# Performance work log

Measured on AMD Instinct MI355X. Metric: run time of the kernel, lower is better.

Reference implementation:

```python
import jax, jax.numpy as jnp
import numpy as np


def setup_inputs() -> dict:
    key = jax.random.key(0)
    ks = jax.random.split(key, 8)
    h = 256
    b, o, T = 64, 64, 50
    s = 1.0 / np.sqrt(h)  # torch LSTM/Linear default init scale
    return {
        "x": jax.random.normal(ks[0], (b, o, h), dtype=jnp.float32),
        "W_ih": jax.random.uniform(ks[1], (4 * h, h), jnp.float32, -s, s),
        "W_hh": jax.random.uniform(ks[2], (4 * h, h), jnp.float32, -s, s),
        "b_ih": jax.random.uniform(ks[3], (4 * h,), jnp.float32, -s, s),
        "b_hh": jax.random.uniform(ks[4], (4 * h,), jnp.float32, -s, s),
        "c0": jnp.zeros((1, h), dtype=jnp.float32),
        "W_out": jax.random.uniform(ks[5], (h, h), jnp.float32, -s, s),
        "b_out": jax.random.uniform(ks[6], (h,), jnp.float32, -s, s),
        "sequence_length": T,
    }


def reference(x, W_ih, W_hh, b_ih, b_hh, c0, W_out, b_out, sequence_length):
    b, o, f = x.shape
    B = b * o
    h0 = x.reshape(B, f)                       # initial hidden state = input
    c_init = jnp.broadcast_to(c0, (B, f))      # learned initial cell state
    # Input token is constant across time: precompute input projection once.
    x_proj = h0 @ W_ih.T + b_ih + b_hh         # (B, 4f)

    def step(carry, _):
        hp, cp = carry
        gates = x_proj + hp @ W_hh.T           # (B, 4f), torch gate order i,f,g,o
        i_g, f_g, g_g, o_g = jnp.split(gates, 4, axis=-1)
        i_g = jax.nn.sigmoid(i_g)
        f_g = jax.nn.sigmoid(f_g)
        g_g = jnp.tanh(g_g)
        o_g = jax.nn.sigmoid(o_g)
        c = f_g * cp + i_g * g_g
        hn = o_g * jnp.tanh(c)
        return (hn, c), hn

    (_, _), hs = jax.lax.scan(step, (h0, c_init), None, length=sequence_length)
    # hs: (T, B, f) -> (b, o, T, f)
    hs = hs.transpose(1, 0, 2).reshape(b, o, sequence_length, f)
    return hs @ W_out.T + b_out
```

## Files before the change

### kernel.cpp

```cpp
#include <hip/hip_runtime.h>

typedef __attribute__((ext_vector_type(8))) short short8;
typedef __attribute__((ext_vector_type(4))) float f32x4;

#define F   256
#define SH  264

__device__ __forceinline__ short f2bf(float f) {
    union { float f; unsigned u; } v; v.f = f;
    unsigned r = (v.u + 0x7fffu + ((v.u >> 16) & 1u)) >> 16;
    return (short)r;
}
__device__ __forceinline__ float bf2f(short s) {
    union { float f; unsigned u; } v; v.u = ((unsigned)(unsigned short)s) << 16;
    return v.f;
}
__device__ __forceinline__ float sigm(float x) {
    return __builtin_amdgcn_rcpf(1.f + __builtin_amdgcn_exp2f(-1.442695041f * x));
}
__device__ __forceinline__ float tanhx(float x) {
    return 1.f - 2.f * __builtin_amdgcn_rcpf(1.f + __builtin_amdgcn_exp2f(2.885390082f * x));
}
__device__ __forceinline__ f32x4 splat4(float v) {
    f32x4 r; r[0] = v; r[1] = v; r[2] = v; r[3] = v; return r;
}

__global__ void pack_kernel(const float* __restrict__ Whh, const float* __restrict__ Wih,
                            const float* __restrict__ Wout,
                            short* __restrict__ whh_p, short* __restrict__ wih_hi,
                            short* __restrict__ wih_lo, short* __restrict__ wout_p)
{
    int idx = blockIdx.x * blockDim.x + threadIdx.x;
    if (idx < 64 * 8 * 64) {
        int lane = idx & 63, kt = (idx >> 6) & 7, nt = idx >> 9;
        int n = nt * 16 + (lane & 15);
        int k = kt * 32 + (lane >> 4) * 8;
        const float* s1 = Whh + n * F + k;
        const float* s2 = Wih + n * F + k;
        #pragma unroll
        for (int j = 0; j < 8; j++) {
            whh_p[idx * 8 + j] = f2bf(s1[j]);
            float v = s2[j];
            short hi = f2bf(v);
            wih_hi[idx * 8 + j] = hi;
            wih_lo[idx * 8 + j] = f2bf(v - bf2f(hi));
        }
    } else {
        int i2 = idx - 64 * 8 * 64;
        if (i2 < 16 * 8 * 64) {
            int lane = i2 & 63, kt = (i2 >> 6) & 7, nt = i2 >> 9;
            int n = nt * 16 + (lane & 15);
            int k = kt * 32 + (lane >> 4) * 8;
            const float* s = Wout + n * F + k;
            #pragma unroll
            for (int j = 0; j < 8; j++) wout_p[i2 * 8 + j] = f2bf(s[j]);
        }
    }
}

__device__ __forceinline__ void gate_mm(f32x4 (&acc)[8][2], const short* __restrict__ Wp,
                                        const short* hb, int w, int lane)
{
    const int l15 = lane & 15, quad = lane >> 4;
    #pragma unroll
    for (int kt = 0; kt < 8; kt++) {
        short8 a0 = *(const short8*)(hb + l15 * SH + kt * 32 + quad * 8);
        short8 a1 = *(const short8*)(hb + (16 + l15) * SH + kt * 32 + quad * 8);
        #pragma unroll
        for (int i = 0; i < 8; i++) {
            int nt = (i >> 1) * 16 + 2 * w + (i & 1);
            short8 b = *(const short8*)(Wp + ((nt * 8 + kt) * 64 + lane) * 8);
            acc[i][0] = __builtin_amdgcn_mfma_f32_16x16x32_bf16(a0, b, acc[i][0], 0, 0, 0);
            acc[i][1] = __builtin_amdgcn_mfma_f32_16x16x32_bf16(a1, b, acc[i][1], 0, 0, 0);
        }
    }
}

__global__ __launch_bounds__(512, 2)
void lstm_fused(const float* __restrict__ x, const float* __restrict__ b_ih,
                const float* __restrict__ b_hh, const float* __restrict__ c0,
                const float* __restrict__ b_out,
                const short* __restrict__ whh_p, const short* __restrict__ wih_hi,
                const short* __restrict__ wih_lo, const short* __restrict__ wout_p,
                const int* __restrict__ seqlen, float* __restrict__ out)
{
    __shared__ short hbuf[32 * SH];
    const int T    = *seqlen;
    const int tid  = threadIdx.x;
    const int lane = tid & 63;
    const int w    = tid >> 6;
    const int l15  = lane & 15;
    const int quad = lane >> 4;
    const int row0 = blockIdx.x * 32;

    const int xr = tid >> 4;
    const int xc = (tid & 15) * 16;
    float xv[16];
    {
        const float* xp = x + (size_t)(row0 + xr) * F + xc;
        #pragma unroll
        for (int j = 0; j < 16; j++) xv[j] = xp[j];
    }

    f32x4 xpj[8][2];
    #pragma unroll
    for (int i = 0; i < 8; i++) { xpj[i][0] = splat4(0.f); xpj[i][1] = splat4(0.f); }

    #pragma unroll
    for (int j = 0; j < 16; j++) {
        short hi = f2bf(xv[j]);
        hbuf[xr * SH + xc + j] = f2bf(xv[j] - bf2f(hi));
    }
    __syncthreads();
    gate_mm(xpj, wih_hi, hbuf, w, lane);
    __syncthreads();
    #pragma unroll
    for (int j = 0; j < 16; j++) hbuf[xr * SH + xc + j] = f2bf(xv[j]);
    __syncthreads();
    gate_mm(xpj, wih_hi, hbuf, w, lane);
    gate_mm(xpj, wih_lo, hbuf, w, lane);

    #pragma unroll
    for (int i = 0; i < 8; i++) {
        int nt = (i >> 1) * 16 + 2 * w + (i & 1);
        float bias = b_ih[nt * 16 + l15] + b_hh[nt * 16 + l15];
        #pragma unroll
        for (int mt = 0; mt < 2; mt++)
            #pragma unroll
            for (int r = 0; r < 4; r++) xpj[i][mt][r] += bias;
    }

    float cst[2][2][4];
    float bo[2];
    #pragma unroll
    for (int s = 0; s < 2; s++) {
        float cv = c0[w * 32 + s * 16 + l15];
        bo[s]    = b_out[w * 32 + s * 16 + l15];
        #pragma unroll
        for (int mt = 0; mt < 2; mt++)
            #pragma unroll
            for (int r = 0; r < 4; r++) cst[s][mt][r] = cv;
    }

    const size_t orow = (size_t)T * F;

    for (int t = 0; t < T; t++) {
        f32x4 acc[8][2];
        #pragma unroll
        for (int i = 0; i < 8; i++) { acc[i][0] = xpj[i][0]; acc[i][1] = xpj[i][1]; }
        gate_mm(acc, whh_p, hbuf, w, lane);

        __syncthreads();

        float hv[2][2][4];
        #pragma unroll
        for (int s = 0; s < 2; s++)
          #pragma unroll
          for (int mt = 0; mt < 2; mt++)
            #pragma unroll
            for (int r = 0; r < 4; r++) {
                float ig = sigm(acc[0 + s][mt][r]);
                float fg = sigm(acc[2 + s][mt][r]);
                float gg = tanhx(acc[4 + s][mt][r]);
                float og = sigm(acc[6 + s][mt][r]);
                float c  = fg * cst[s][mt][r] + ig * gg;
                cst[s][mt][r] = c;
                float h  = og * tanhx(c);
                hv[s][mt][r] = h;
                hbuf[(mt * 16 + quad * 4 + r) * SH + w * 32 + s * 16 + l15] = f2bf(h);
            }
        __syncthreads();

        f32x4 oacc[2][2];
        #pragma unroll
        for (int s = 0; s < 2; s++) { oacc[s][0] = splat4(bo[s]); oacc[s][1] = splat4(bo[s]); }
        #pragma unroll
        for (int kt = 0; kt < 8; kt++) {
            short8 a0 = *(const short8*)(hbuf + l15 * SH + kt * 32 + quad * 8);
            short8 a1 = *(const short8*)(hbuf + (16 + l15) * SH + kt * 32 + quad * 8);
            #pragma unroll
            for (int s = 0; s < 2; s++) {
                int nt = 2 * w + s;
                short8 b = *(const short8*)(wout_p + ((nt * 8 + kt) * 64 + lane) * 8);
                oacc[s][0] = __builtin_amdgcn_mfma_f32_16x16x32_bf16(a0, b, oacc[s][0], 0, 0, 0);
                oacc[s][1] = __builtin_amdgcn_mfma_f32_16x16x32_bf16(a1, b, oacc[s][1], 0, 0, 0);
            }
        }
        float* op = out + (size_t)row0 * orow + (size_t)t * F;
        #pragma unroll
        for (int s = 0; s < 2; s++)
          #pragma unroll
          for (int mt = 0; mt < 2; mt++)
            #pragma unroll
            for (int r = 0; r < 4; r++)
                op[(size_t)(mt * 16 + quad * 4 + r) * orow + w * 32 + s * 16 + l15]
                    = oacc[s][mt][r];
    }
}

extern "C" void kernel_launch(void* const* d_in, const int* in_sizes, int n_in,
                              void* d_out, int out_size, void* d_ws, size_t ws_size,
                              hipStream_t stream)
{
    const float* x    = (const float*)d_in[0];
    const float* Wih  = (const float*)d_in[1];
    const float* Whh  = (const float*)d_in[2];
    const float* bih  = (const float*)d_in[3];
    const float* bhh  = (const float*)d_in[4];
    const float* c0   = (const float*)d_in[5];
    const float* Wout = (const float*)d_in[6];
    const float* bout = (const float*)d_in[7];
    const int* seqlen = (const int*)d_in[8];

    short* whh_p  = (short*)d_ws;
    short* wih_hi = whh_p  + 1024 * 256;
    short* wih_lo = wih_hi + 1024 * 256;
    short* wout_p = wih_lo + 1024 * 256;
    (void)ws_size; (void)in_sizes; (void)n_in; (void)out_size;

    pack_kernel<<<160, 256, 0, stream>>>(Whh, Wih, Wout, whh_p, wih_hi, wih_lo, wout_p);
    lstm_fused<<<128, 512, 0, stream>>>(x, bih, bhh, c0, bout,
                                        whh_p, wih_hi, wih_lo, wout_p,
                                        seqlen, (float*)d_out);
}
```

Baseline: 1.211 ms.

## Split LSTM block across 16 waves and store h in MFMA-fragment LDS layout

Doubles the block to 1024 threads so each of 16 waves owns one 16-column tile per gate instead of two, halving per-wave MFMA work and register pressure on the serial recurrence. The hidden-state LDS buffer is laid out directly in MFMA A-operand fragment order, so A reads become contiguous short8 loads with no padding. Input and output traffic now use nontemporal loads and stores. In exchange there is more barrier cost per step across twice as many waves, and the scattered per-element writes into the fragment-ordered buffer may cause LDS bank conflicts.

```diff
diff --git a/kernel.cpp b/kernel.cpp
--- a/kernel.cpp
+++ b/kernel.cpp
@@ -2,9 +2,9 @@
 
 typedef __attribute__((ext_vector_type(8))) short short8;
 typedef __attribute__((ext_vector_type(4))) float f32x4;
-
-#define F   256
-#define SH  264
+typedef __attribute__((ext_vector_type(4))) float float4v;
+
+#define F 256
 
 __device__ __forceinline__ short f2bf(float f) {
     union { float f; unsigned u; } v; v.f = f;
@@ -58,25 +58,24 @@
     }
 }
 
-__device__ __forceinline__ void gate_mm(f32x4 (&acc)[8][2], const short* __restrict__ Wp,
-                                        const short* hb, int w, int lane)
-{
-    const int l15 = lane & 15, quad = lane >> 4;
+__device__ __forceinline__ void gate_mm16(f32x4 (&acc)[4][2], const short* __restrict__ Wp,
+                                          const short* hb, int w, int lane)
+{
     #pragma unroll
     for (int kt = 0; kt < 8; kt++) {
-        short8 a0 = *(const short8*)(hb + l15 * SH + kt * 32 + quad * 8);
-        short8 a1 = *(const short8*)(hb + (16 + l15) * SH + kt * 32 + quad * 8);
-        #pragma unroll
-        for (int i = 0; i < 8; i++) {
-            int nt = (i >> 1) * 16 + 2 * w + (i & 1);
+        short8 a0 = *(const short8*)(hb + (kt * 64 + lane) * 8);
+        short8 a1 = *(const short8*)(hb + ((8 + kt) * 64 + lane) * 8);
+        #pragma unroll
+        for (int g = 0; g < 4; g++) {
+            int nt = g * 16 + w;
             short8 b = *(const short8*)(Wp + ((nt * 8 + kt) * 64 + lane) * 8);
-            acc[i][0] = __builtin_amdgcn_mfma_f32_16x16x32_bf16(a0, b, acc[i][0], 0, 0, 0);
-            acc[i][1] = __builtin_amdgcn_mfma_f32_16x16x32_bf16(a1, b, acc[i][1], 0, 0, 0);
-        }
-    }
-}
-
-__global__ __launch_bounds__(512, 2)
+            acc[g][0] = __builtin_amdgcn_mfma_f32_16x16x32_bf16(a0, b, acc[g][0], 0, 0, 0);
+            acc[g][1] = __builtin_amdgcn_mfma_f32_16x16x32_bf16(a1, b, acc[g][1], 0, 0, 0);
+        }
+    }
+}
+
+__global__ __launch_bounds__(1024)
 void lstm_fused(const float* __restrict__ x, const float* __restrict__ b_ih,
                 const float* __restrict__ b_hh, const float* __restrict__ c0,
                 const float* __restrict__ b_out,
@@ -84,7 +83,7 @@
                 const short* __restrict__ wih_lo, const short* __restrict__ wout_p,
                 const int* __restrict__ seqlen, float* __restrict__ out)
 {
-    __shared__ short hbuf[32 * SH];
+    __shared__ short hbuf[2 * 8 * 64 * 8];
     const int T    = *seqlen;
     const int tid  = threadIdx.x;
     const int lane = tid & 63;
@@ -93,108 +92,105 @@
     const int quad = lane >> 4;
     const int row0 = blockIdx.x * 32;
 
-    const int xr = tid >> 4;
-    const int xc = (tid & 15) * 16;
-    float xv[16];
+    const int xr = tid >> 5;
+    const int xc = (tid & 31) * 8;
+    float xv[8];
     {
-        const float* xp = x + (size_t)(row0 + xr) * F + xc;
-        #pragma unroll
-        for (int j = 0; j < 16; j++) xv[j] = xp[j];
-    }
-
-    f32x4 xpj[8][2];
-    #pragma unroll
-    for (int i = 0; i < 8; i++) { xpj[i][0] = splat4(0.f); xpj[i][1] = splat4(0.f); }
-
-    #pragma unroll
-    for (int j = 0; j < 16; j++) {
-        short hi = f2bf(xv[j]);
-        hbuf[xr * SH + xc + j] = f2bf(xv[j] - bf2f(hi));
+        const float4v* xp = (const float4v*)(x + (size_t)(row0 + xr) * F + xc);
+        float4v v0 = __builtin_nontemporal_load(xp);
+        float4v v1 = __builtin_nontemporal_load(xp + 1);
+        #pragma unroll
+        for (int j = 0; j < 4; j++) { xv[j] = v0[j]; xv[4 + j] = v1[j]; }
+    }
+    short* xst = hbuf + (size_t)(xr >> 4) * 4096 + ((tid & 31) >> 2) * 512
+                      + ((tid & 31) & 3) * 128 + (xr & 15) * 8;
+
+    f32x4 xpj[4][2];
+    #pragma unroll
+    for (int g = 0; g < 4; g++) { xpj[g][0] = splat4(0.f); xpj[g][1] = splat4(0.f); }
+
+    {
+        short8 s;
+        #pragma unroll
+        for (int j = 0; j < 8; j++) { short hi = f2bf(xv[j]); s[j] = f2bf(xv[j] - bf2f(hi)); }
+        *(short8*)xst = s;
     }
     __syncthreads();
-    gate_mm(xpj, wih_hi, hbuf, w, lane);
+    gate_mm16(xpj, wih_hi, hbuf, w, lane);
     __syncthreads();
-    #pragma unroll
-    for (int j = 0; j < 16; j++) hbuf[xr * SH + xc + j] = f2bf(xv[j]);
+    {
+        short8 s;
+        #pragma unroll
+        for (int j = 0; j < 8; j++) s[j] = f2bf(xv[j]);
+        *(short8*)xst = s;
+    }
     __syncthreads();
-    gate_mm(xpj, wih_hi, hbuf, w, lane);
-    gate_mm(xpj, wih_lo, hbuf, w, lane);
-
-    #pragma unroll
-    for (int i = 0; i < 8; i++) {
-        int nt = (i >> 1) * 16 + 2 * w + (i & 1);
-        float bias = b_ih[nt * 16 + l15] + b_hh[nt * 16 + l15];
+    gate_mm16(xpj, wih_hi, hbuf, w, lane);
+    gate_mm16(xpj, wih_lo, hbuf, w, lane);
+
+    #pragma unroll
+    for (int g = 0; g < 4; g++) {
+        int n = g * 256 + w * 16 + l15;
+        float bias = b_ih[n] + b_hh[n];
         #pragma unroll
         for (int mt = 0; mt < 2; mt++)
             #pragma unroll
-            for (int r = 0; r < 4; r++) xpj[i][mt][r] += bias;
-    }
-
-    float cst[2][2][4];
-    float bo[2];
-    #pragma unroll
-    for (int s = 0; s < 2; s++) {
-        float cv = c0[w * 32 + s * 16 + l15];
-        bo[s]    = b_out[w * 32 + s * 16 + l15];
+            for (int r = 0; r < 4; r++) xpj[g][mt][r] += bias;
+    }
+
+    const int hcol = w * 16 + l15;
+    float cst[2][4];
+    const float cv = c0[hcol];
+    const float bo = b_out[hcol];
+    #pragma unroll
+    for (int mt = 0; mt < 2; mt++)
+        #pragma unroll
+        for (int r = 0; r < 4; r++) cst[mt][r] = cv;
+
+    const int hoff = (hcol >> 5) * 512 + ((hcol >> 3) & 3) * 128 + (hcol & 7) + quad * 32;
+
+    const size_t orow = (size_t)T * F;
+    float* obase = out + (size_t)row0 * orow + hcol;
+
+    for (int t = 0; t < T; t++) {
+        f32x4 acc[4][2];
+        #pragma unroll
+        for (int g = 0; g < 4; g++) { acc[g][0] = xpj[g][0]; acc[g][1] = xpj[g][1]; }
+        gate_mm16(acc, whh_p, hbuf, w, lane);
+
+        __syncthreads();
+
         #pragma unroll
         for (int mt = 0; mt < 2; mt++)
             #pragma unroll
-            for (int r = 0; r < 4; r++) cst[s][mt][r] = cv;
-    }
-
-    const size_t orow = (size_t)T * F;
-
-    for (int t = 0; t < T; t++) {
-        f32x4 acc[8][2];
-        #pragma unroll
-        for (int i = 0; i < 8; i++) { acc[i][0] = xpj[i][0]; acc[i][1] = xpj[i][1]; }
-        gate_mm(acc, whh_p, hbuf, w, lane);
-
-        __syncthreads();
-
-        float hv[2][2][4];
-        #pragma unroll
-        for (int s = 0; s < 2; s++)
-          #pragma unroll
-          for (int mt = 0; mt < 2; mt++)
-            #pragma unroll
             for (int r = 0; r < 4; r++) {
-                float ig = sigm(acc[0 + s][mt][r]);
-                float fg = sigm(acc[2 + s][mt][r]);
-                float gg = tanhx(acc[4 + s][mt][r]);
-                float og = sigm(acc[6 + s][mt][r]);
-                float c  = fg * cst[s][mt][r] + ig * gg;
-                cst[s][mt][r] = c;
-                float h  = og * tanhx(c);
-                hv[s][mt][r] = h;
-                hbuf[(mt * 16 + quad * 4 + r) * SH + w * 32 + s * 16 + l15] = f2bf(h);
+                float ig = sigm(acc[0][mt][r]);
+                float fg = sigm(acc[1][mt][r]);
+                float gg = tanhx(acc[2][mt][r]);
+                float og = sigm(acc[3][mt][r]);
+                float c  = fg * cst[mt][r] + ig * gg;
+                cst[mt][r] = c;
+                hbuf[mt * 4096 + hoff + r * 8] = f2bf(og * tanhx(c));
             }
         __syncthreads();
 
-        f32x4 oacc[2][2];
-        #pragma unroll
-        for (int s = 0; s < 2; s++) { oacc[s][0] = splat4(bo[s]); oacc[s][1] = splat4(bo[s]); }
+        f32x4 oacc[2];
+        oacc[0] = splat4(bo); oacc[1] = splat4(bo);
         #pragma unroll
         for (int kt = 0; kt < 8; kt++) {
-            short8 a0 = *(const short8*)(hbuf + l15 * SH + kt * 32 + quad * 8);
-            short8 a1 = *(const short8*)(hbuf + (16 + l15) * SH + kt * 32 + quad * 8);
-            #pragma unroll
-            for (int s = 0; s < 2; s++) {
-                int nt = 2 * w + s;
-                short8 b = *(const short8*)(wout_p + ((nt * 8 + kt) * 64 + lane) * 8);
-                oacc[s][0] = __builtin_amdgcn_mfma_f32_16x16x32_bf16(a0, b, oacc[s][0], 0, 0, 0);
-                oacc[s][1] = __builtin_amdgcn_mfma_f32_16x16x32_bf16(a1, b, oacc[s][1], 0, 0, 0);
-            }
-        }
-        float* op = out + (size_t)row0 * orow + (size_t)t * F;
-        #pragma unroll
-        for (int s = 0; s < 2; s++)
-          #pragma unroll
-          for (int mt = 0; mt < 2; mt++)
+            short8 a0 = *(const short8*)(hbuf + (kt * 64 + lane) * 8);
+            short8 a1 = *(const short8*)(hbuf + ((8 + kt) * 64 + lane) * 8);
+            short8 b  = *(const short8*)(wout_p + ((w * 8 + kt) * 64 + lane) * 8);
+            oacc[0] = __builtin_amdgcn_mfma_f32_16x16x32_bf16(a0, b, oacc[0], 0, 0, 0);
+            oacc[1] = __builtin_amdgcn_mfma_f32_16x16x32_bf16(a1, b, oacc[1], 0, 0, 0);
+        }
+        float* op = obase + (size_t)t * F;
+        #pragma unroll
+        for (int mt = 0; mt < 2; mt++)
             #pragma unroll
             for (int r = 0; r < 4; r++)
-                op[(size_t)(mt * 16 + quad * 4 + r) * orow + w * 32 + s * 16 + l15]
-                    = oacc[s][mt][r];
+                __builtin_nontemporal_store(oacc[mt][r],
+                    op + (size_t)(mt * 16 + quad * 4 + r) * orow);
     }
 }
 
@@ -219,7 +215,7 @@
     (void)ws_size; (void)in_sizes; (void)n_in; (void)out_size;
 
     pack_kernel<<<160, 256, 0, stream>>>(Whh, Wih, Wout, whh_p, wih_hi, wih_lo, wout_p);
-    lstm_fused<<<128, 512, 0, stream>>>(x, bih, bhh, c0, bout,
-                                        whh_p, wih_hi, wih_lo, wout_p,
-                                        seqlen, (float*)d_out);
-}
+    lstm_fused<<<128, 1024, 0, stream>>>(x, bih, bhh, c0, bout,
+                                         whh_p, wih_hi, wih_lo, wout_p,
+                                         seqlen, (float*)d_out);
+}
```

New measurement: 1.537 ms. +27.0%, slower.
